# Performance work log

Measured on AMD Instinct MI355X. Metric: run time of the kernel, lower is better.

## Reference

```python
import jax, jax.numpy as jnp
import numpy as np
import math

DIM = 1024
NHEADS = 8
HEAD_DIM = 128
MAXSEQLEN = 2048
THETA = 10000.0


def _rope_tables():
    # speed = theta ** (-(arange(0, dim, 2) / dim)), t = arange(maxseqlen)
    half = HEAD_DIM // 2
    speed = THETA ** (-(np.arange(0, HEAD_DIM, 2)[:half].astype(np.float32) / HEAD_DIM))
    t = np.arange(MAXSEQLEN, dtype=np.float32)
    freqs = np.outer(t, speed)  # [maxseqlen, head_dim//2]
    return jnp.asarray(np.cos(freqs)), jnp.asarray(np.sin(freqs))


def setup_inputs() -> dict:
    key = jax.random.key(0)
    kx, kqkv, kout = jax.random.split(key, 3)
    B, T = 2, 2048
    hdim = NHEADS * HEAD_DIM
    std = 0.5 * DIM ** (-0.5)
    bound = (3.0 ** 0.5) * std
    x = jax.random.normal(kx, (B, T, DIM), dtype=jnp.float32)
    qkv_proj = jax.random.uniform(kqkv, (3, hdim, DIM), dtype=jnp.float32,
                                  minval=-bound, maxval=bound)
    # nn.Linear(hdim, dim, bias=False) default init: U(-1/sqrt(hdim), 1/sqrt(hdim))
    wb = 1.0 / math.sqrt(hdim)
    w_out = jax.random.uniform(kout, (DIM, hdim), dtype=jnp.float32,
                               minval=-wb, maxval=wb)
    cos, sin = _rope_tables()
    return {"x": x, "qkv_proj": qkv_proj, "w_out": w_out, "cos": cos, "sin": sin}


def _apply_rope(u, cos, sin):
    # u: [B, T, H, D]; rotate adjacent pairs (complex multiply)
    B, T, H, D = u.shape
    u = u.reshape(B, T, H, D // 2, 2)
    c = cos[:T][None, :, None, :]  # [1, T, 1, D//2]
    s = sin[:T][None, :, None, :]
    re = u[..., 0] * c - u[..., 1] * s
    im = u[..., 0] * s + u[..., 1] * c
    return jnp.stack([re, im], axis=-1).reshape(B, T, H, D)


def reference(x, qkv_proj, w_out, cos, sin):
    B, T, D = x.shape
    # fused QKV projection: [B, T, 3, hdim] -> [B, T, 3, H, head_dim]
    qkv = jnp.einsum('btd,ahd->btah', x, qkv_proj)
    qkv = qkv.reshape(B, T, 3, NHEADS, HEAD_DIM)
    q, k, v = qkv[:, :, 0], qkv[:, :, 1], qkv[:, :, 2]
    q = _apply_rope(q, cos, sin)
    k = _apply_rope(k, cos, sin)
    scale = HEAD_DIM ** (-0.5)
    logits = jnp.einsum('btnh,bsnh->bnts', q, k) * scale  # [B, H, T, T]
    causal = jnp.tril(jnp.ones((T, T), dtype=bool))
    masked = jnp.where(causal[None, None], logits, -jnp.inf)
    attn = jax.nn.softmax(masked, axis=-1)
    out = jnp.einsum('bnts,bsnh->btnh', attn, v).reshape(B, T, -1)
    out = out @ w_out.T  # [B, T, dim]
    return out, attn
```

## Files before the change

kernel.cpp:

```cpp
#include <hip/hip_runtime.h>

typedef __attribute__((ext_vector_type(8))) short bf16x8;
typedef __attribute__((ext_vector_type(4))) short bf16x4;
typedef __attribute__((ext_vector_type(4))) float f32x4;

#define MFMA(a, b, c) __builtin_amdgcn_mfma_f32_16x16x32_bf16((a), (b), (c), 0, 0, 0)

__device__ __forceinline__ unsigned short f2bf(float f) {
  unsigned int x = __float_as_uint(f);
  return (unsigned short)((x + 0x7fffu + ((x >> 16) & 1u)) >> 16);
}
__device__ __forceinline__ unsigned int cvtpk(float lo, float hi) {
  unsigned int r;
  asm("v_cvt_pk_bf16_f32 %0, %1, %2" : "=v"(r) : "v"(lo), "v"(hi));
  return r;
}

constexpr int SEQ = 2048;
constexpr int NH = 8;
constexpr int DH = 128;
constexpr int DIM = 1024;
constexpr float SCALE = 0.08838834764831845f;

__global__ __launch_bounds__(256) void k_qkv_rope(
    const float* __restrict__ x, const float* __restrict__ wqkv,
    const float* __restrict__ cosT, const float* __restrict__ sinT,
    unsigned short* __restrict__ q, unsigned short* __restrict__ k,
    unsigned short* __restrict__ vT)
{
  __shared__ __align__(16) unsigned short As[128][40];
  __shared__ __align__(16) unsigned short Bs[128][40];
  const int tid = threadIdx.x;
  const int wave = tid >> 6, lane = tid & 63;
  const int fr = lane & 15, fq = lane >> 4;
  const int fk = fq * 8;
  const int wr = (wave >> 1) * 64, wc = (wave & 1) * 64;
  const int m0 = blockIdx.x * 128, n0 = blockIdx.y * 128;

  f32x4 zero4 = {0.f, 0.f, 0.f, 0.f};
  f32x4 acc[4][4];
  for (int i = 0; i < 4; ++i)
    for (int j = 0; j < 4; ++j) acc[i][j] = zero4;

  for (int kt = 0; kt < 32; ++kt) {
    const int k0 = kt * 32;
    __syncthreads();
#pragma unroll
    for (int j = 0; j < 4; ++j) {
      int f = j * 256 + tid;
      int row = f >> 3, c4 = (f & 7) * 4;
      f32x4 va = *(const f32x4*)(x + (m0 + row) * 1024 + k0 + c4);
      f32x4 vb = *(const f32x4*)(wqkv + (n0 + row) * 1024 + k0 + c4);
      uint2 ua, ub;
      ua.x = cvtpk(va[0], va[1]); ua.y = cvtpk(va[2], va[3]);
      ub.x = cvtpk(vb[0], vb[1]); ub.y = cvtpk(vb[2], vb[3]);
      *(uint2*)&As[row][c4] = ua;
      *(uint2*)&Bs[row][c4] = ub;
    }
    __syncthreads();
    bf16x8 af[4], bfr[4];
#pragma unroll
    for (int mi = 0; mi < 4; ++mi) af[mi] = *(const bf16x8*)&As[wr + mi * 16 + fr][fk];
#pragma unroll
    for (int ni = 0; ni < 4; ++ni) bfr[ni] = *(const bf16x8*)&Bs[wc + ni * 16 + fr][fk];
#pragma unroll
    for (int mi = 0; mi < 4; ++mi)
#pragma unroll
      for (int ni = 0; ni < 4; ++ni)
        acc[mi][ni] = MFMA(af[mi], bfr[ni], acc[mi][ni]);
  }

#pragma unroll
  for (int mi = 0; mi < 4; ++mi)
#pragma unroll
    for (int ni = 0; ni < 4; ++ni)
#pragma unroll
      for (int r = 0; r < 4; ++r) {
        float val = acc[mi][ni][r];
        float other = __shfl_xor(val, 1, 64);
        int m = m0 + wr + mi * 16 + fq * 4 + r;
        int n = n0 + wc + ni * 16 + fr;
        int a = n >> 10, feat = n & 1023;
        int hh = feat >> 7, dh = feat & 127;
        int bi = m >> 11, t = m & 2047;
        if (a == 2) {
          vT[((bi * NH + hh) * DH + dh) * SEQ + t] = f2bf(val);
        } else {
          float c = cosT[t * 64 + (dh >> 1)];
          float s = sinT[t * 64 + (dh >> 1)];
          float o = ((dh & 1) == 0) ? (val * c - other * s) : (other * s + val * c);
          unsigned short* dst = (a == 0) ? q : k;
          dst[((bi * NH + hh) * SEQ + t) * DH + dh] = f2bf(o);
        }
      }
}

__global__ __launch_bounds__(256) void k_attn(
    const unsigned short* __restrict__ q, const unsigned short* __restrict__ k,
    const unsigned short* __restrict__ vT,
    float* __restrict__ attn, unsigned short* __restrict__ heads)
{
  __shared__ __align__(16) unsigned short Kt[128][136];
  __shared__ __align__(16) unsigned short Vt[128][132];

  const int tid = threadIdx.x;
  const int wave = tid >> 6, lane = tid & 63;
  const int fr = lane & 15, fq = lane >> 4;
  const int fk = fq * 8;
  const int rt = (blockIdx.z == 0) ? (int)blockIdx.x : (31 - (int)blockIdx.x);
  const int row0 = rt * 64;
  const int hh = blockIdx.y, bi = blockIdx.z;
  const int bh = bi * NH + hh;
  const int r0 = row0 + wave * 16;
  const int wmax = r0 + 15;
  const int myrow = r0 + fr;

  const unsigned short* qb = q + bh * SEQ * DH;
  const unsigned short* kb = k + bh * SEQ * DH;
  const unsigned short* vb = vT + bh * DH * SEQ;

  bf16x8 aq[4];
#pragma unroll
  for (int ks = 0; ks < 4; ++ks)
    aq[ks] = *(const bf16x8*)(qb + myrow * DH + ks * 32 + fk);

  const int nph = (rt + 2) >> 1;
  float rs = 0.f;

  for (int ph = 0; ph < nph; ++ph) {
    const int c0 = ph * 128;
    __syncthreads();
#pragma unroll
    for (int j = 0; j < 8; ++j) {
      int f = j * 256 + tid;
      int r = f >> 4, c = (f & 15) * 8;
      *(bf16x8*)&Kt[r][c] = *(const bf16x8*)(kb + (c0 + r) * DH + c);
    }
    __syncthreads();
#pragma unroll
    for (int half = 0; half < 8; ++half) {
      int ch = c0 + half * 16;
      if (ch <= wmax) {
        f32x4 s = {0.f, 0.f, 0.f, 0.f};
#pragma unroll
        for (int ks = 0; ks < 4; ++ks) {
          bf16x8 bk = *(const bf16x8*)&Kt[half * 16 + fr][ks * 32 + fk];
          s = MFMA(bk, aq[ks], s);
        }
#pragma unroll
        for (int r = 0; r < 4; ++r) {
          int col = ch + fq * 4 + r;
          if (col <= myrow) rs += __expf(s[r] * SCALE);
        }
      }
    }
  }

  rs += __shfl_xor(rs, 16, 64);
  rs += __shfl_xor(rs, 32, 64);
  const float inv = 1.0f / rs;

  f32x4 pv[8];
  {
    f32x4 zero4 = {0.f, 0.f, 0.f, 0.f};
#pragma unroll
    for (int i = 0; i < 8; ++i) pv[i] = zero4;
  }

  for (int ph = 0; ph < nph; ++ph) {
    const int c0 = ph * 128;
    __syncthreads();
#pragma unroll
    for (int j = 0; j < 8; ++j) {
      int f = j * 256 + tid;
      int r = f >> 4, c = (f & 15) * 8;
      *(bf16x8*)&Kt[r][c] = *(const bf16x8*)(kb + (c0 + r) * DH + c);
      bf16x8 w = *(const bf16x8*)(vb + r * SEQ + c0 + c);
      int cb = c & ~31, within = c & 31;
      int s8 = (within >> 3) & 1, b0 = within >> 4;
      int col0 = cb + 16 * s8 + 4 * b0;
      bf16x4 lo = {w[0], w[1], w[2], w[3]};
      bf16x4 hi = {w[4], w[5], w[6], w[7]};
      *(bf16x4*)&Vt[r][col0] = lo;
      *(bf16x4*)&Vt[r][col0 + 8] = hi;
    }
    __syncthreads();
#pragma unroll
    for (int chunk = 0; chunk < 4; ++chunk) {
      union { unsigned int u[4]; bf16x8 v8; } pa;
#pragma unroll
      for (int h2 = 0; h2 < 2; ++h2) {
        const int half = chunk * 2 + h2;
        const int ch = c0 + half * 16;
        const bool live = (ch <= wmax);
        f32x4 s = {0.f, 0.f, 0.f, 0.f};
        if (live) {
#pragma unroll
          for (int ks = 0; ks < 4; ++ks) {
            bf16x8 bk = *(const bf16x8*)&Kt[half * 16 + fr][ks * 32 + fk];
            s = MFMA(bk, aq[ks], s);
          }
        }
        float p[4];
#pragma unroll
        for (int r = 0; r < 4; ++r) {
          int col = ch + fq * 4 + r;
          p[r] = (live && col <= myrow) ? __expf(s[r] * SCALE) * inv : 0.f;
        }
        f32x4 p4 = {p[0], p[1], p[2], p[3]};
        __builtin_nontemporal_store(
            p4, (f32x4*)(attn + ((size_t)bh * SEQ + myrow) * SEQ + ch + fq * 4));
        pa.u[h2 * 2] = cvtpk(p[0], p[1]);
        pa.u[h2 * 2 + 1] = cvtpk(p[2], p[3]);
      }
#pragma unroll
      for (int ni = 0; ni < 8; ++ni) {
        bf16x8 bv = *(const bf16x8*)&Vt[ni * 16 + fr][chunk * 32 + fq * 8];
        pv[ni] = MFMA(pa.v8, bv, pv[ni]);
      }
    }
  }

#pragma unroll
  for (int ni = 0; ni < 8; ++ni)
#pragma unroll
    for (int r = 0; r < 4; ++r) {
      int row = r0 + fq * 4 + r;
      int dh = ni * 16 + fr;
      heads[(bi * SEQ + row) * DIM + hh * DH + dh] = f2bf(pv[ni][r]);
    }

  {
    const int zstart = nph * 128;
    f32x4 z4 = {0.f, 0.f, 0.f, 0.f};
#pragma unroll
    for (int rr = 0; rr < 4; ++rr) {
      int row = r0 + rr * 4 + fq;
      float* dst = attn + ((size_t)bh * SEQ + row) * SEQ;
      for (int c = zstart + fr * 4; c < SEQ; c += 64)
        __builtin_nontemporal_store(z4, (f32x4*)(dst + c));
    }
  }
}

__global__ __launch_bounds__(256) void k_outproj(
    const unsigned short* __restrict__ heads, const float* __restrict__ wout,
    float* __restrict__ out)
{
  __shared__ __align__(16) unsigned short As[128][40];
  __shared__ __align__(16) unsigned short Bs[128][40];
  const int tid = threadIdx.x;
  const int wave = tid >> 6, lane = tid & 63;
  const int fr = lane & 15, fq = lane >> 4;
  const int fk = fq * 8;
  const int wr = (wave >> 1) * 64, wc = (wave & 1) * 64;
  const int m0 = blockIdx.x * 128, n0 = blockIdx.y * 128;

  f32x4 zero4 = {0.f, 0.f, 0.f, 0.f};
  f32x4 acc[4][4];
  for (int i = 0; i < 4; ++i)
    for (int j = 0; j < 4; ++j) acc[i][j] = zero4;

  for (int kt = 0; kt < 32; ++kt) {
    const int k0 = kt * 32;
    __syncthreads();
#pragma unroll
    for (int j = 0; j < 2; ++j) {
      int f = j * 256 + tid;
      int row = f >> 2, c = (f & 3) * 8;
      *(bf16x8*)&As[row][c] = *(const bf16x8*)(heads + (m0 + row) * 1024 + k0 + c);
    }
#pragma unroll
    for (int j = 0; j < 4; ++j) {
      int f = j * 256 + tid;
      int row = f >> 3, c4 = (f & 7) * 4;
      f32x4 vb = *(const f32x4*)(wout + (n0 + row) * 1024 + k0 + c4);
      uint2 ub;
      ub.x = cvtpk(vb[0], vb[1]); ub.y = cvtpk(vb[2], vb[3]);
      *(uint2*)&Bs[row][c4] = ub;
    }
    __syncthreads();
    bf16x8 af[4], bfr[4];
#pragma unroll
    for (int mi = 0; mi < 4; ++mi) af[mi] = *(const bf16x8*)&As[wr + mi * 16 + fr][fk];
#pragma unroll
    for (int ni = 0; ni < 4; ++ni) bfr[ni] = *(const bf16x8*)&Bs[wc + ni * 16 + fr][fk];
#pragma unroll
    for (int mi = 0; mi < 4; ++mi)
#pragma unroll
      for (int ni = 0; ni < 4; ++ni)
        acc[mi][ni] = MFMA(af[mi], bfr[ni], acc[mi][ni]);
  }

#pragma unroll
  for (int mi = 0; mi < 4; ++mi)
#pragma unroll
    for (int ni = 0; ni < 4; ++ni)
#pragma unroll
      for (int r = 0; r < 4; ++r) {
        int m = m0 + wr + mi * 16 + fq * 4 + r;
        int n = n0 + wc + ni * 16 + fr;
        out[m * 1024 + n] = acc[mi][ni][r];
      }
}

extern "C" void kernel_launch(void* const* d_in, const int* in_sizes, int n_in,
                              void* d_out, int out_size, void* d_ws, size_t ws_size,
                              hipStream_t stream)
{
  const float* x    = (const float*)d_in[0];
  const float* wqkv = (const float*)d_in[1];
  const float* wout = (const float*)d_in[2];
  const float* cosT = (const float*)d_in[3];
  const float* sinT = (const float*)d_in[4];

  float* out  = (float*)d_out;
  float* attn = out + 4194304;
  unsigned short* ws = (unsigned short*)d_ws;
  unsigned short* q     = ws;
  unsigned short* kk    = ws + 4194304;
  unsigned short* vT    = ws + 8388608;
  unsigned short* heads = ws + 12582912;

  k_qkv_rope<<<dim3(32, 24), 256, 0, stream>>>(x, wqkv, cosT, sinT, q, kk, vT);
  k_attn<<<dim3(32, 8, 2), 256, 0, stream>>>(q, kk, vT, attn, heads);
  k_outproj<<<dim3(32, 8), 256, 0, stream>>>(heads, wout, out);
}
```

Measured before the change: 210.5 us.

## Fuse softmax into a single pass with deferred row normalization via bf16 staging

Drops the first QK^T pass that only computed row sums. Unnormalized exp values are now accumulated into PV, and the row sums are gathered as a side effect. The exp values are staged as bf16 in the first half of each attention output row, then a final pass reads them back, scales them by the inverse row sum and writes fp32 probabilities, including the zero tail. This halves the MFMA and K-load work but adds a global read-back of the staged band. It also lowers the precision of the attention output to bf16-rounded values, and there is no max subtraction, which relies on logits staying small.

```diff
diff --git a/kernel.cpp b/kernel.cpp
--- a/kernel.cpp
+++ b/kernel.cpp
@@ -9,6 +9,9 @@
 __device__ __forceinline__ unsigned short f2bf(float f) {
   unsigned int x = __float_as_uint(f);
   return (unsigned short)((x + 0x7fffu + ((x >> 16) & 1u)) >> 16);
+}
+__device__ __forceinline__ float bf2f(unsigned short u) {
+  return __uint_as_float(((unsigned int)u) << 16);
 }
 __device__ __forceinline__ unsigned int cvtpk(float lo, float hi) {
   unsigned int r;
@@ -102,6 +105,7 @@
 {
   __shared__ __align__(16) unsigned short Kt[128][136];
   __shared__ __align__(16) unsigned short Vt[128][132];
+  __shared__ float invs[64];
 
   const int tid = threadIdx.x;
   const int wave = tid >> 6, lane = tid & 63;
@@ -127,45 +131,15 @@
   const int nph = (rt + 2) >> 1;
   float rs = 0.f;
 
-  for (int ph = 0; ph < nph; ++ph) {
-    const int c0 = ph * 128;
-    __syncthreads();
-#pragma unroll
-    for (int j = 0; j < 8; ++j) {
-      int f = j * 256 + tid;
-      int r = f >> 4, c = (f & 15) * 8;
-      *(bf16x8*)&Kt[r][c] = *(const bf16x8*)(kb + (c0 + r) * DH + c);
-    }
-    __syncthreads();
-#pragma unroll
-    for (int half = 0; half < 8; ++half) {
-      int ch = c0 + half * 16;
-      if (ch <= wmax) {
-        f32x4 s = {0.f, 0.f, 0.f, 0.f};
-#pragma unroll
-        for (int ks = 0; ks < 4; ++ks) {
-          bf16x8 bk = *(const bf16x8*)&Kt[half * 16 + fr][ks * 32 + fk];
-          s = MFMA(bk, aq[ks], s);
-        }
-#pragma unroll
-        for (int r = 0; r < 4; ++r) {
-          int col = ch + fq * 4 + r;
-          if (col <= myrow) rs += __expf(s[r] * SCALE);
-        }
-      }
-    }
-  }
-
-  rs += __shfl_xor(rs, 16, 64);
-  rs += __shfl_xor(rs, 32, 64);
-  const float inv = 1.0f / rs;
-
   f32x4 pv[8];
   {
     f32x4 zero4 = {0.f, 0.f, 0.f, 0.f};
 #pragma unroll
     for (int i = 0; i < 8; ++i) pv[i] = zero4;
   }
+
+  unsigned short* bandRow =
+      (unsigned short*)attn + (((size_t)bh * SEQ + myrow) * SEQ) * 2;
 
   for (int ph = 0; ph < nph; ++ph) {
     const int c0 = ph * 128;
@@ -205,13 +179,15 @@
 #pragma unroll
         for (int r = 0; r < 4; ++r) {
           int col = ch + fq * 4 + r;
-          p[r] = (live && col <= myrow) ? __expf(s[r] * SCALE) * inv : 0.f;
+          p[r] = (live && col <= myrow) ? __expf(s[r] * SCALE) : 0.f;
         }
-        f32x4 p4 = {p[0], p[1], p[2], p[3]};
-        __builtin_nontemporal_store(
-            p4, (f32x4*)(attn + ((size_t)bh * SEQ + myrow) * SEQ + ch + fq * 4));
+        rs += (p[0] + p[1]) + (p[2] + p[3]);
         pa.u[h2 * 2] = cvtpk(p[0], p[1]);
         pa.u[h2 * 2 + 1] = cvtpk(p[2], p[3]);
+        uint2 bw;
+        bw.x = pa.u[h2 * 2];
+        bw.y = pa.u[h2 * 2 + 1];
+        *(uint2*)(bandRow + ch + fq * 4) = bw;
       }
 #pragma unroll
       for (int ni = 0; ni < 8; ++ni) {
@@ -221,24 +197,58 @@
     }
   }
 
+  rs += __shfl_xor(rs, 16, 64);
+  rs += __shfl_xor(rs, 32, 64);
+  if (fq == 0) invs[wave * 16 + fr] = 1.0f / rs;
+  __syncthreads();
+
+  float invr[4];
+#pragma unroll
+  for (int r = 0; r < 4; ++r) invr[r] = invs[wave * 16 + fq * 4 + r];
 #pragma unroll
   for (int ni = 0; ni < 8; ++ni)
 #pragma unroll
     for (int r = 0; r < 4; ++r) {
       int row = r0 + fq * 4 + r;
       int dh = ni * 16 + fr;
-      heads[(bi * SEQ + row) * DIM + hh * DH + dh] = f2bf(pv[ni][r]);
+      heads[(bi * SEQ + row) * DIM + hh * DH + dh] = f2bf(pv[ni][r] * invr[r]);
     }
 
   {
-    const int zstart = nph * 128;
-    f32x4 z4 = {0.f, 0.f, 0.f, 0.f};
-#pragma unroll
-    for (int rr = 0; rr < 4; ++rr) {
-      int row = r0 + rr * 4 + fq;
-      float* dst = attn + ((size_t)bh * SEQ + row) * SEQ;
-      for (int c = zstart + fr * 4; c < SEQ; c += 64)
-        __builtin_nontemporal_store(z4, (f32x4*)(dst + c));
+    const int erow = row0 + (tid >> 2);
+    const float rinv = invs[tid >> 2];
+    const int sub = (tid & 3) * 128;
+    const int W = nph * 128;
+    unsigned short* brow =
+        (unsigned short*)attn + (((size_t)bh * SEQ + erow) * SEQ) * 2;
+    float* frow = attn + ((size_t)bh * SEQ + erow) * SEQ;
+#pragma unroll
+    for (int qd = 3; qd >= 0; --qd) {
+      const int base = qd * 512 + sub;
+      const bool in = (base < W);
+      bf16x8 buf[16];
+      if (in) {
+#pragma unroll
+        for (int i = 0; i < 16; ++i)
+          buf[i] = *(const bf16x8*)&brow[base + i * 8];
+      }
+      asm volatile("s_waitcnt vmcnt(0)" ::: "memory");
+#pragma unroll
+      for (int i = 0; i < 16; ++i) {
+        f32x4 w0 = {0.f, 0.f, 0.f, 0.f}, w1 = {0.f, 0.f, 0.f, 0.f};
+        if (in) {
+          w0[0] = bf2f((unsigned short)buf[i][0]) * rinv;
+          w0[1] = bf2f((unsigned short)buf[i][1]) * rinv;
+          w0[2] = bf2f((unsigned short)buf[i][2]) * rinv;
+          w0[3] = bf2f((unsigned short)buf[i][3]) * rinv;
+          w1[0] = bf2f((unsigned short)buf[i][4]) * rinv;
+          w1[1] = bf2f((unsigned short)buf[i][5]) * rinv;
+          w1[2] = bf2f((unsigned short)buf[i][6]) * rinv;
+          w1[3] = bf2f((unsigned short)buf[i][7]) * rinv;
+        }
+        __builtin_nontemporal_store(w0, (f32x4*)(frow + base + i * 8));
+        __builtin_nontemporal_store(w1, (f32x4*)(frow + base + i * 8 + 4));
+      }
     }
   }
 }
```

New measurement: 756.1 us. +259.3%, slower.
